# Kernel optimization log

Hardware: AMD Instinct MI355X
Metric: run time of the kernel (lower is better)

The kernel has to match this reference:

```python
import jax, jax.numpy as jnp
import numpy as np

B, IN_F, OUT_F, KD = 256, 1024, 128, 16


def setup_inputs() -> dict:
    key = jax.random.key(0)
    k1, k2 = jax.random.split(key)
    x = jax.random.normal(k1, (B, IN_F), dtype=jnp.float32)
    t_mat = jax.random.normal(k2, (IN_F, OUT_F, KD), dtype=jnp.float32)
    return {"x": x, "t_mat": t_mat}


def reference(x, t_mat):
    # Projection: [B, in] @ [in, out*kd] -> [B, out, kd]
    m = jnp.einsum('bi,iok->bok', x, t_mat)
    # All-pairs L1 distance over kernel dim: [B, B, out]
    norm = jnp.sum(jnp.abs(m[:, None, :, :] - m[None, :, :, :]), axis=-1)
    # exp(-norm) summed over the partner axis; subtract 1 for self-pair (norm=0 -> exp=1)
    o_b = jnp.sum(jnp.exp(-norm), axis=1) - 1.0  # [B, out]
    return jnp.concatenate([x, o_b], axis=1)  # [B, in + out]
```

## Files before the change

### kernel.cpp

```cpp
#include <hip/hip_runtime.h>
#include <hip/hip_fp16.h>


#define BATCH 256
#define INF   1024
#define OUTF  128
#define KDIM  16
#define TCOLS 2048
#define OCOLS 1152
#define XB    1032

typedef __attribute__((ext_vector_type(8))) short short8;
typedef __attribute__((ext_vector_type(4))) float f32x4;
typedef __attribute__((ext_vector_type(4))) unsigned short ushort4v;

__device__ inline unsigned short bf_trunc(float f) {
    return (unsigned short)(__float_as_uint(f) >> 16);
}

__global__ __launch_bounds__(256) void k_prep(const float* __restrict__ x,
                                              unsigned short* __restrict__ xs) {
    const int i = blockIdx.x * 256 + threadIdx.x;
    float4 v = reinterpret_cast<const float4*>(x)[i];
    ushort4v o = { bf_trunc(v.x), bf_trunc(v.y), bf_trunc(v.z), bf_trunc(v.w) };
    reinterpret_cast<ushort4v*>(xs)[i] = o;
}

__global__ __launch_bounds__(1024, 4) void k_fused(const float* __restrict__ x,
                                                   const float* __restrict__ T,
                                                   const unsigned short* __restrict__ xs,
                                                   float* __restrict__ out) {
    const int blk = blockIdx.x;
    const int o   = blk & 127;
    const int h   = blk >> 7;
    const int tid = threadIdx.x;
    const int wave = tid >> 6, lane = tid & 63;
    const int l15 = lane & 15, q = lane >> 4;

    __shared__ unsigned short bs[16][XB];
    __shared__ __half2 pm[BATCH][8];
    __shared__ float part[32][128];

    if (tid < 256)
        reinterpret_cast<float4*>(out)[blk * 288 + tid] =
            reinterpret_cast<const float4*>(x)[blk * 256 + tid];

    {
        const int kb = tid >> 2, n0 = (tid & 3) * 4;
        float4 tv[4];
        #pragma unroll
        for (int pass = 0; pass < 4; ++pass)
            tv[pass] = *reinterpret_cast<const float4*>(
                &T[(pass * 256 + kb) * TCOLS + o * KDIM + n0]);
        #pragma unroll
        for (int pass = 0; pass < 4; ++pass) {
            const int k = pass * 256 + kb;
            bs[n0 + 0][k] = bf_trunc(tv[pass].x);
            bs[n0 + 1][k] = bf_trunc(tv[pass].y);
            bs[n0 + 2][k] = bf_trunc(tv[pass].z);
            bs[n0 + 3][k] = bf_trunc(tv[pass].w);
        }
    }
    __syncthreads();

    const unsigned short* xr = xs + (wave * 16 + l15) * INF + q * 8;

    f32x4 acc = {0.f, 0.f, 0.f, 0.f};
    {
        short8 a[16];
        #pragma unroll
        for (int i = 0; i < 16; ++i)
            a[i] = *reinterpret_cast<const short8*>(xr + i * 32);
        __builtin_amdgcn_sched_barrier(0);
        #pragma unroll
        for (int ks = 0; ks < 16; ++ks) {
            short8 bfr = *reinterpret_cast<const short8*>(&bs[l15][ks * 32 + q * 8]);
            acc = __builtin_amdgcn_mfma_f32_16x16x32_bf16(a[ks], bfr, acc, 0, 0, 0);
        }
        #pragma unroll
        for (int i = 0; i < 16; ++i)
            a[i] = *reinterpret_cast<const short8*>(xr + (16 + i) * 32);
        __builtin_amdgcn_sched_barrier(0);
        #pragma unroll
        for (int ks = 0; ks < 16; ++ks) {
            short8 bfr = *reinterpret_cast<const short8*>(&bs[l15][(16 + ks) * 32 + q * 8]);
            acc = __builtin_amdgcn_mfma_f32_16x16x32_bf16(a[ks], bfr, acc, 0, 0, 0);
        }
    }

    {
        __half* pmh = reinterpret_cast<__half*>(pm);
        #pragma unroll
        for (int r = 0; r < 4; ++r)
            pmh[(wave * 16 + q * 4 + r) * 16 + l15] = __float2half(acc[r]);
    }
    __syncthreads();

    const int i1 = tid & 31;
    const int bsel = tid >> 5;
    __half2 my[4][8];
    #pragma unroll
    for (int r = 0; r < 4; ++r) {
        union { uint4 u[2]; __half2 hh[8]; } c;
        c.u[0] = *reinterpret_cast<const uint4*>(&pm[h * 128 + r * 32 + i1][0]);
        c.u[1] = *reinterpret_cast<const uint4*>(&pm[h * 128 + r * 32 + i1][4]);
        #pragma unroll
        for (int j = 0; j < 8; ++j) my[r][j] = c.hh[j];
    }

    float tot[4] = {0.f, 0.f, 0.f, 0.f};
    const int b2_lo = bsel * 8;
    #pragma unroll
    for (int b2 = b2_lo; b2 < b2_lo + 8; ++b2) {
        union { uint4 u[2]; __half2 hh[8]; } co;
        co.u[0] = *reinterpret_cast<const uint4*>(&pm[b2][0]);
        co.u[1] = *reinterpret_cast<const uint4*>(&pm[b2][4]);
        #pragma unroll
        for (int r = 0; r < 4; ++r) {
            __half2 e0 = __habs2(__hsub2(my[r][0], co.hh[0]));
            __half2 e1 = __habs2(__hsub2(my[r][1], co.hh[1]));
            __half2 e2 = __habs2(__hsub2(my[r][2], co.hh[2]));
            __half2 e3 = __habs2(__hsub2(my[r][3], co.hh[3]));
            e0 = __hadd2(e0, __habs2(__hsub2(my[r][4], co.hh[4])));
            e1 = __hadd2(e1, __habs2(__hsub2(my[r][5], co.hh[5])));
            e2 = __hadd2(e2, __habs2(__hsub2(my[r][6], co.hh[6])));
            e3 = __hadd2(e3, __habs2(__hsub2(my[r][7], co.hh[7])));
            __half2 es = __hadd2(__hadd2(e0, e1), __hadd2(e2, e3));
            float n = __low2float(es) + __high2float(es);
            tot[r] += __expf(-n);
        }
    }
    #pragma unroll
    for (int r = 0; r < 4; ++r)
        part[bsel][r * 32 + i1] = tot[r];
    __syncthreads();

    if (tid < 128) {
        float s = -1.0f;
        #pragma unroll
        for (int j = 0; j < 32; ++j) s += part[j][tid];
        out[(h * 128 + tid) * OCOLS + INF + o] = s;
    }
}

extern "C" void kernel_launch(void* const* d_in, const int* in_sizes, int n_in,
                              void* d_out, int out_size, void* d_ws, size_t ws_size,
                              hipStream_t stream) {
    const float* x = (const float*)d_in[0];
    const float* T = (const float*)d_in[1];
    float* out = (float*)d_out;
    unsigned short* xs = (unsigned short*)d_ws;

    k_prep<<<256, 256, 0, stream>>>(x, xs);
    k_fused<<<256, 1024, 0, stream>>>(x, T, xs, out);
}
```

Baseline: 86.74 us.

## Move x copy to prep, double-buffer A loads, pad pm, tree-reduce partials

The copy of x into the output moves from the fused kernel into the prep kernel. The A-fragment global loads are split into two 8-register buffers so loads overlap the MFMAs. The pm shared array row stride is padded to reduce LDS bank conflicts. The pairwise loop prefetches the next partner row, and the final 32-way partial sum becomes a two-level reduction across more threads. Together these target load latency, bank conflicts and the serial reduction tail, at the cost of extra syncs and some register pressure.

Result: no change. 86.74 us (-0.0%).

```diff
diff --git a/kernel.cpp b/kernel.cpp
--- a/kernel.cpp
+++ b/kernel.cpp
@@ -9,6 +9,7 @@
 #define TCOLS 2048
 #define OCOLS 1152
 #define XB    1032
+#define PMW   12
 
 typedef __attribute__((ext_vector_type(8))) short short8;
 typedef __attribute__((ext_vector_type(4))) float f32x4;
@@ -19,15 +20,17 @@
 }
 
 __global__ __launch_bounds__(256) void k_prep(const float* __restrict__ x,
-                                              unsigned short* __restrict__ xs) {
-    const int i = blockIdx.x * 256 + threadIdx.x;
+                                              unsigned short* __restrict__ xs,
+                                              float* __restrict__ out) {
+    const int b = blockIdx.x, t = threadIdx.x;
+    const int i = b * 256 + t;
     float4 v = reinterpret_cast<const float4*>(x)[i];
-    ushort4v o = { bf_trunc(v.x), bf_trunc(v.y), bf_trunc(v.z), bf_trunc(v.w) };
-    reinterpret_cast<ushort4v*>(xs)[i] = o;
+    ushort4v o4 = { bf_trunc(v.x), bf_trunc(v.y), bf_trunc(v.z), bf_trunc(v.w) };
+    reinterpret_cast<ushort4v*>(xs)[i] = o4;
+    reinterpret_cast<float4*>(out)[b * 288 + t] = v;
 }
 
-__global__ __launch_bounds__(1024, 4) void k_fused(const float* __restrict__ x,
-                                                   const float* __restrict__ T,
+__global__ __launch_bounds__(1024, 4) void k_fused(const float* __restrict__ T,
                                                    const unsigned short* __restrict__ xs,
                                                    float* __restrict__ out) {
     const int blk = blockIdx.x;
@@ -38,12 +41,8 @@
     const int l15 = lane & 15, q = lane >> 4;
 
     __shared__ unsigned short bs[16][XB];
-    __shared__ __half2 pm[BATCH][8];
+    __shared__ __half2 pm[BATCH][PMW];
     __shared__ float part[32][128];
-
-    if (tid < 256)
-        reinterpret_cast<float4*>(out)[blk * 288 + tid] =
-            reinterpret_cast<const float4*>(x)[blk * 256 + tid];
 
     {
         const int kb = tid >> 2, n0 = (tid & 3) * 4;
@@ -67,24 +66,36 @@
 
     f32x4 acc = {0.f, 0.f, 0.f, 0.f};
     {
-        short8 a[16];
+        short8 A[8], Bb[8];
         #pragma unroll
-        for (int i = 0; i < 16; ++i)
-            a[i] = *reinterpret_cast<const short8*>(xr + i * 32);
+        for (int i = 0; i < 8; ++i) A[i]  = *reinterpret_cast<const short8*>(xr + i * 32);
+        #pragma unroll
+        for (int i = 0; i < 8; ++i) Bb[i] = *reinterpret_cast<const short8*>(xr + (8 + i) * 32);
         __builtin_amdgcn_sched_barrier(0);
+
         #pragma unroll
-        for (int ks = 0; ks < 16; ++ks) {
+        for (int ks = 0; ks < 8; ++ks) {
             short8 bfr = *reinterpret_cast<const short8*>(&bs[l15][ks * 32 + q * 8]);
-            acc = __builtin_amdgcn_mfma_f32_16x16x32_bf16(a[ks], bfr, acc, 0, 0, 0);
+            acc = __builtin_amdgcn_mfma_f32_16x16x32_bf16(A[ks], bfr, acc, 0, 0, 0);
         }
         #pragma unroll
-        for (int i = 0; i < 16; ++i)
-            a[i] = *reinterpret_cast<const short8*>(xr + (16 + i) * 32);
-        __builtin_amdgcn_sched_barrier(0);
+        for (int i = 0; i < 8; ++i) A[i] = *reinterpret_cast<const short8*>(xr + (16 + i) * 32);
         #pragma unroll
-        for (int ks = 0; ks < 16; ++ks) {
-            short8 bfr = *reinterpret_cast<const short8*>(&bs[l15][(16 + ks) * 32 + q * 8]);
-            acc = __builtin_amdgcn_mfma_f32_16x16x32_bf16(a[ks], bfr, acc, 0, 0, 0);
+        for (int ks = 8; ks < 16; ++ks) {
+            short8 bfr = *reinterpret_cast<const short8*>(&bs[l15][ks * 32 + q * 8]);
+            acc = __builtin_amdgcn_mfma_f32_16x16x32_bf16(Bb[ks - 8], bfr, acc, 0, 0, 0);
+        }
+        #pragma unroll
+        for (int i = 0; i < 8; ++i) Bb[i] = *reinterpret_cast<const short8*>(xr + (24 + i) * 32);
+        #pragma unroll
+        for (int ks = 16; ks < 24; ++ks) {
+            short8 bfr = *reinterpret_cast<const short8*>(&bs[l15][ks * 32 + q * 8]);
+            acc = __builtin_amdgcn_mfma_f32_16x16x32_bf16(A[ks - 16], bfr, acc, 0, 0, 0);
+        }
+        #pragma unroll
+        for (int ks = 24; ks < 32; ++ks) {
+            short8 bfr = *reinterpret_cast<const short8*>(&bs[l15][ks * 32 + q * 8]);
+            acc = __builtin_amdgcn_mfma_f32_16x16x32_bf16(Bb[ks - 24], bfr, acc, 0, 0, 0);
         }
     }
 
@@ -92,7 +103,7 @@
         __half* pmh = reinterpret_cast<__half*>(pm);
         #pragma unroll
         for (int r = 0; r < 4; ++r)
-            pmh[(wave * 16 + q * 4 + r) * 16 + l15] = __float2half(acc[r]);
+            pmh[(wave * 16 + q * 4 + r) * (2 * PMW) + l15] = __float2half(acc[r]);
     }
     __syncthreads();
 
@@ -108,23 +119,46 @@
         for (int j = 0; j < 8; ++j) my[r][j] = c.hh[j];
     }
 
+    union U16 { uint4 u[2]; __half2 hh[8]; };
     float tot[4] = {0.f, 0.f, 0.f, 0.f};
     const int b2_lo = bsel * 8;
+
+    U16 c0, c1;
+    c0.u[0] = *reinterpret_cast<const uint4*>(&pm[b2_lo][0]);
+    c0.u[1] = *reinterpret_cast<const uint4*>(&pm[b2_lo][4]);
+
     #pragma unroll
-    for (int b2 = b2_lo; b2 < b2_lo + 8; ++b2) {
-        union { uint4 u[2]; __half2 hh[8]; } co;
-        co.u[0] = *reinterpret_cast<const uint4*>(&pm[b2][0]);
-        co.u[1] = *reinterpret_cast<const uint4*>(&pm[b2][4]);
+    for (int ib = 0; ib < 8; ib += 2) {
+        c1.u[0] = *reinterpret_cast<const uint4*>(&pm[b2_lo + ib + 1][0]);
+        c1.u[1] = *reinterpret_cast<const uint4*>(&pm[b2_lo + ib + 1][4]);
         #pragma unroll
         for (int r = 0; r < 4; ++r) {
-            __half2 e0 = __habs2(__hsub2(my[r][0], co.hh[0]));
-            __half2 e1 = __habs2(__hsub2(my[r][1], co.hh[1]));
-            __half2 e2 = __habs2(__hsub2(my[r][2], co.hh[2]));
-            __half2 e3 = __habs2(__hsub2(my[r][3], co.hh[3]));
-            e0 = __hadd2(e0, __habs2(__hsub2(my[r][4], co.hh[4])));
-            e1 = __hadd2(e1, __habs2(__hsub2(my[r][5], co.hh[5])));
-            e2 = __hadd2(e2, __habs2(__hsub2(my[r][6], co.hh[6])));
-            e3 = __hadd2(e3, __habs2(__hsub2(my[r][7], co.hh[7])));
+            __half2 e0 = __habs2(__hsub2(my[r][0], c0.hh[0]));
+            __half2 e1 = __habs2(__hsub2(my[r][1], c0.hh[1]));
+            __half2 e2 = __habs2(__hsub2(my[r][2], c0.hh[2]));
+            __half2 e3 = __habs2(__hsub2(my[r][3], c0.hh[3]));
+            e0 = __hadd2(e0, __habs2(__hsub2(my[r][4], c0.hh[4])));
+            e1 = __hadd2(e1, __habs2(__hsub2(my[r][5], c0.hh[5])));
+            e2 = __hadd2(e2, __habs2(__hsub2(my[r][6], c0.hh[6])));
+            e3 = __hadd2(e3, __habs2(__hsub2(my[r][7], c0.hh[7])));
+            __half2 es = __hadd2(__hadd2(e0, e1), __hadd2(e2, e3));
+            float n = __low2float(es) + __high2float(es);
+            tot[r] += __expf(-n);
+        }
+        if (ib + 2 < 8) {
+            c0.u[0] = *reinterpret_cast<const uint4*>(&pm[b2_lo + ib + 2][0]);
+            c0.u[1] = *reinterpret_cast<const uint4*>(&pm[b2_lo + ib + 2][4]);
+        }
+        #pragma unroll
+        for (int r = 0; r < 4; ++r) {
+            __half2 e0 = __habs2(__hsub2(my[r][0], c1.hh[0]));
+            __half2 e1 = __habs2(__hsub2(my[r][1], c1.hh[1]));
+            __half2 e2 = __habs2(__hsub2(my[r][2], c1.hh[2]));
+            __half2 e3 = __habs2(__hsub2(my[r][3], c1.hh[3]));
+            e0 = __hadd2(e0, __habs2(__hsub2(my[r][4], c1.hh[4])));
+            e1 = __hadd2(e1, __habs2(__hsub2(my[r][5], c1.hh[5])));
+            e2 = __hadd2(e2, __habs2(__hsub2(my[r][6], c1.hh[6])));
+            e3 = __hadd2(e3, __habs2(__hsub2(my[r][7], c1.hh[7])));
             __half2 es = __hadd2(__hadd2(e0, e1), __hadd2(e2, e3));
             float n = __low2float(es) + __high2float(es);
             tot[r] += __expf(-n);
@@ -135,10 +169,18 @@
         part[bsel][r * 32 + i1] = tot[r];
     __syncthreads();
 
+    {
+        const int g = tid >> 7, b1 = tid & 127;
+        float s = part[g * 4 + 0][b1] + part[g * 4 + 1][b1]
+                + part[g * 4 + 2][b1] + part[g * 4 + 3][b1];
+        __syncthreads();
+        part[g * 4][b1] = s;
+    }
+    __syncthreads();
     if (tid < 128) {
         float s = -1.0f;
         #pragma unroll
-        for (int j = 0; j < 32; ++j) s += part[j][tid];
+        for (int g = 0; g < 8; ++g) s += part[g * 4][tid];
         out[(h * 128 + tid) * OCOLS + INF + o] = s;
     }
 }
@@ -151,6 +193,6 @@
     float* out = (float*)d_out;
     unsigned short* xs = (unsigned short*)d_ws;
 
-    k_prep<<<256, 256, 0, stream>>>(x, xs);
-    k_fused<<<256, 1024, 0, stream>>>(x, T, xs, out);
+    k_prep<<<256, 256, 0, stream>>>(x, xs, out);
+    k_fused<<<256, 1024, 0, stream>>>(T, xs, out);
 }
```
